# Optimization experiments

Measured on AMD Instinct MI355X. Metric: run time of the kernel, lower is better.

Reference implementation:

```python
import jax, jax.numpy as jnp
import numpy as np


def conv2d_same(x, w, b):
    # x: (B,C,H,W), w: (O,I,3,3) -> 3x3 'same' conv, stride 1
    y = jax.lax.conv_general_dilated(
        x, w, window_strides=(1, 1), padding=((1, 1), (1, 1)),
        dimension_numbers=("NCHW", "OIHW", "NCHW"))
    return y + b[None, :, None, None]


def setup_inputs() -> dict:
    key = jax.random.key(0)
    ks = jax.random.split(key, 7)
    B, F, E, H, W = 16, 64, 16, 64, 64
    fan2d = F * 9
    state = jax.random.normal(ks[0], (B, F, H, W), dtype=jnp.float32)
    pre_w = jax.random.normal(ks[1], (F, F, 3, 3), dtype=jnp.float32) / np.sqrt(fan2d)
    pre_b = jax.random.normal(ks[2], (F,), dtype=jnp.float32) * 0.01
    attn_w = jax.random.normal(ks[3], (E, F, 3, 3), dtype=jnp.float32) / np.sqrt(fan2d)
    attn_b = jax.random.normal(ks[4], (E,), dtype=jnp.float32) * 0.01
    c3_w = jax.random.normal(ks[5], (F, F), dtype=jnp.float32) / np.sqrt(F)
    c3_b = jax.random.normal(ks[6], (F,), dtype=jnp.float32) * 0.01
    return {"state": state, "pre_w": pre_w, "pre_b": pre_b,
            "attn_w": attn_w, "attn_b": attn_b, "c3_w": c3_w, "c3_b": c3_b}


def reference(state, pre_w, pre_b, attn_w, attn_b, c3_w, c3_b):
    # pre_conv + relu
    x = jax.nn.relu(conv2d_same(state, pre_w, pre_b))
    # visattn_conv + sigmoid -> (B,E,H,W)
    attn = jax.nn.sigmoid(conv2d_same(x, attn_w, attn_b))
    # einsum 'bfyx,beyx->bfeyx'
    x5 = state[:, :, None, :, :] * attn[:, None, :, :, :]  # (B,F,E,H,W)
    # Conv3d kernel (1,1,1) with padding (0,1,1): zero-pad H,W by 1,
    # then pointwise linear over F. Output spatial dims become (E, H+2, W+2).
    x5 = jnp.pad(x5, ((0, 0), (0, 0), (0, 0), (1, 1), (1, 1)))
    y = jnp.einsum("of,bfeyx->boeyx", c3_w, x5) + c3_b[None, :, None, None, None]
    y = jax.nn.relu(y)
    # permute (0,2,1,3,4) then mean over last two dims -> (B,E,F)
    out = jnp.mean(y, axis=(-1, -2)).transpose(0, 2, 1)
    return out, attn
```

## Files before the change

kernel.cpp:

```cpp
#include <hip/hip_runtime.h>
#include <math.h>

constexpr int B = 16, F = 64, E = 16, H = 64, W = 64;
constexpr int HW = H * W;
constexpr int XP = 66;
constexpr int CP = 72;
constexpr int YSTRIDE = XP * F;

typedef __bf16 bf16x8 __attribute__((ext_vector_type(8)));
typedef __bf16 bf16x4 __attribute__((ext_vector_type(4)));
typedef float f32x16 __attribute__((ext_vector_type(16)));
typedef float f32x4 __attribute__((ext_vector_type(4)));

__global__ __launch_bounds__(256) void prep_kernel(
    const float* __restrict__ state, const float* __restrict__ pre_w,
    const float* __restrict__ attn_w, const float* __restrict__ c3_w,
    __bf16* __restrict__ xTs, __bf16* __restrict__ wA1,
    __bf16* __restrict__ wA2, __bf16* __restrict__ wT3b,
    float* __restrict__ out0)
{
    __shared__ float s_t[64][68];
    const int blk = blockIdx.x;
    const int tid = threadIdx.x;

    if (blk < 1024) {
        const int b = blk >> 6, y = blk & 63;
        {
            int c = tid >> 2, x0 = (tid & 3) * 16;
            const float* src = state + ((size_t)(b * F + c) * H + y) * W + x0;
            #pragma unroll
            for (int q = 0; q < 4; ++q)
                *(float4*)&s_t[c][x0 + 4 * q] = *(const float4*)(src + 4 * q);
        }
        __syncthreads();
        __bf16* dst = xTs + (size_t)(b * H + y) * YSTRIDE;
        #pragma unroll
        for (int i = 0; i < 2; ++i) {
            int t = tid + i * 256;
            int x = t >> 3, cg = t & 7;
            bf16x8 v;
            #pragma unroll
            for (int j = 0; j < 8; ++j) v[j] = (__bf16)s_t[cg * 8 + j][x];
            *(bf16x8*)(dst + (x + 1) * F + cg * 8) = v;
        }
        if (tid < 16) {
            int bd = tid >> 3, cg = tid & 7;
            bf16x8 z = {};
            *(bf16x8*)(dst + (bd ? 65 : 0) * F + cg * 8) = z;
        }
    } else if (blk < 1168) {
        int idx = (blk - 1024) * 256 + tid;
        if (idx < 64 * 576) {
            int o = idx / 576, rem = idx - o * 576, t = rem >> 6, c = rem & 63;
            wA1[idx] = (__bf16)pre_w[(o * 64 + c) * 9 + t];
        }
        if (idx < 16 * 576) {
            int e = idx / 576, rem = idx - e * 576, t = rem >> 6, c = rem & 63;
            wA2[idx] = (__bf16)attn_w[(e * 64 + c) * 9 + t];
        }
        if (idx < 64 * 64) {
            wT3b[idx] = (__bf16)c3_w[idx];
        }
    } else {
        int idx = (blk - 1168) * 256 + tid;
        float4 z = {0.f, 0.f, 0.f, 0.f};
        *(float4*)(out0 + idx * 4) = z;
    }
}

__global__ __launch_bounds__(256) void conv1_mfma(
    const __bf16* __restrict__ xTs, const __bf16* __restrict__ wA1,
    const float* __restrict__ bias, __bf16* __restrict__ xT1)
{
    __shared__ __bf16 s_x[4 * XP * CP];
    const int b = blockIdx.y, y0 = blockIdx.x * 2;
    const int tid = threadIdx.x;

    for (int t = tid; t < 4 * XP * 8; t += 256) {
        int r = t / (XP * 8);
        int rem = t - r * (XP * 8);
        int x = rem >> 3, cg = rem & 7;
        int yy = y0 - 1 + r;
        bf16x8 v = {};
        if (yy >= 0 && yy < H)
            v = *(const bf16x8*)(xTs + (size_t)(b * H + yy) * YSTRIDE + x * F + cg * 8);
        *(bf16x8*)(s_x + (r * XP + x) * CP + cg * 8) = v;
    }
    __syncthreads();

    const int wave = tid >> 6, lane = tid & 63;
    const int mt = wave & 1;
    const int np = wave >> 1;
    const int n = lane & 31, kh = lane >> 5;
    f32x16 acc0 = {}, acc1 = {};
    const __bf16* aBase = wA1 + (mt * 32 + n) * 576 + kh * 8;

    #pragma unroll
    for (int dy = 0; dy < 3; ++dy) {
        #pragma unroll
        for (int dx = 0; dx < 3; ++dx) {
            const int t9 = dy * 3 + dx;
            const __bf16* bBase = s_x + ((np + dy) * XP + (n + dx)) * CP + kh * 8;
            #pragma unroll
            for (int cq = 0; cq < 4; ++cq) {
                bf16x8 a  = *(const bf16x8*)(aBase + t9 * 64 + cq * 16);
                bf16x8 b0 = *(const bf16x8*)(bBase + cq * 16);
                bf16x8 b1 = *(const bf16x8*)(bBase + 32 * CP + cq * 16);
                acc0 = __builtin_amdgcn_mfma_f32_32x32x16_bf16(a, b0, acc0, 0, 0, 0);
                acc1 = __builtin_amdgcn_mfma_f32_32x32x16_bf16(a, b1, acc1, 0, 0, 0);
            }
        }
    }

    __bf16* obase = xT1 + (size_t)(b * H + y0 + np) * YSTRIDE;
    #pragma unroll
    for (int g = 0; g < 4; ++g) {
        int o0 = mt * 32 + kh * 4 + g * 8;
        f32x4 b4 = *(const f32x4*)(bias + o0);
        bf16x4 v0, v1;
        #pragma unroll
        for (int r = 0; r < 4; ++r) {
            v0[r] = (__bf16)fmaxf(acc0[g * 4 + r] + b4[r], 0.f);
            v1[r] = (__bf16)fmaxf(acc1[g * 4 + r] + b4[r], 0.f);
        }
        *(bf16x4*)(obase + (n + 1) * F + o0) = v0;
        *(bf16x4*)(obase + (n + 33) * F + o0) = v1;
    }
    if (tid < 32) {
        int r2 = tid >> 4, bd = (tid >> 3) & 1, cg = tid & 7;
        bf16x8 z = {};
        *(bf16x8*)(xT1 + (size_t)(b * H + y0 + r2) * YSTRIDE + (bd ? 65 : 0) * F + cg * 8) = z;
    }
}

__global__ __launch_bounds__(256) void conv2_mfma(
    const __bf16* __restrict__ xT1, const __bf16* __restrict__ wA2,
    const float* __restrict__ bias, float* __restrict__ attn)
{
    __shared__ __bf16 s_x[6 * XP * CP];
    const int b = blockIdx.y, y0 = blockIdx.x * 4;
    const int tid = threadIdx.x;

    for (int t = tid; t < 6 * XP * 8; t += 256) {
        int r = t / (XP * 8);
        int rem = t - r * (XP * 8);
        int x = rem >> 3, cg = rem & 7;
        int yy = y0 - 1 + r;
        bf16x8 v = {};
        if (yy >= 0 && yy < H)
            v = *(const bf16x8*)(xT1 + (size_t)(b * H + yy) * YSTRIDE + x * F + cg * 8);
        *(bf16x8*)(s_x + (r * XP + x) * CP + cg * 8) = v;
    }
    __syncthreads();

    const int w = tid >> 6, lane = tid & 63;
    const int n = lane & 15, quad = lane >> 4;
    f32x4 acc[4] = {};
    const __bf16* aBase = wA2 + n * 576 + quad * 8;

    #pragma unroll
    for (int dy = 0; dy < 3; ++dy) {
        #pragma unroll
        for (int dx = 0; dx < 3; ++dx) {
            const int t9 = dy * 3 + dx;
            const __bf16* bBase = s_x + ((w + dy) * XP + (n + dx)) * CP + quad * 8;
            #pragma unroll
            for (int cq = 0; cq < 2; ++cq) {
                bf16x8 a = *(const bf16x8*)(aBase + t9 * 64 + cq * 32);
                #pragma unroll
                for (int i = 0; i < 4; ++i) {
                    bf16x8 bf = *(const bf16x8*)(bBase + (i * 16) * CP + cq * 32);
                    acc[i] = __builtin_amdgcn_mfma_f32_16x16x32_bf16(a, bf, acc[i], 0, 0, 0);
                }
            }
        }
    }

    const int y = y0 + w;
    #pragma unroll
    for (int i = 0; i < 4; ++i) {
        int x = i * 16 + n;
        #pragma unroll
        for (int r = 0; r < 4; ++r) {
            int e = quad * 4 + r;
            float val = acc[i][r] + bias[e];
            attn[((size_t)(b * E + e) * H + y) * W + x] = 1.f / (1.f + __expf(-val));
        }
    }
}

__global__ __launch_bounds__(256) void reduce_fused(
    const __bf16* __restrict__ xTs, const __bf16* __restrict__ wT3b,
    const float* __restrict__ attn, const float* __restrict__ c3_b,
    float* __restrict__ out)
{
    __shared__ __align__(16) float s_attn[64][16];
    __shared__ __align__(16) float s_sp[64][68];
    const int b = blockIdx.y, y = blockIdx.x;
    const int tid = threadIdx.x;

    {
        int e = tid >> 4, pq = (tid & 15) * 4;
        float4 v = *(const float4*)(attn + ((size_t)(b * E + e) * H + y) * W + pq);
        s_attn[pq + 0][e] = v.x; s_attn[pq + 1][e] = v.y;
        s_attn[pq + 2][e] = v.z; s_attn[pq + 3][e] = v.w;
    }

    {
        const int wave = tid >> 6, lane = tid & 63;
        const int mt = wave & 1, nt = wave >> 1;
        const int n = lane & 31, kh = lane >> 5;
        const __bf16* bBase = xTs + (size_t)(b * H + y) * YSTRIDE + (nt * 32 + n + 1) * F + kh * 8;
        const __bf16* aBase = wT3b + (mt * 32 + n) * 64 + kh * 8;
        f32x16 acc = {};
        #pragma unroll
        for (int cq = 0; cq < 4; ++cq) {
            bf16x8 a  = *(const bf16x8*)(aBase + cq * 16);
            bf16x8 bb = *(const bf16x8*)(bBase + cq * 16);
            acc = __builtin_amdgcn_mfma_f32_32x32x16_bf16(a, bb, acc, 0, 0, 0);
        }
        #pragma unroll
        for (int g = 0; g < 4; ++g)
            #pragma unroll
            for (int r = 0; r < 4; ++r)
                s_sp[nt * 32 + n][mt * 32 + kh * 4 + g * 8 + r] = acc[g * 4 + r];
    }
    __syncthreads();

    const int combo = tid & 63;
    const int eg = combo >> 4;
    const int og = combo & 15;
    const int psub = tid >> 6;
    float4 cb4 = ((const float4*)c3_b)[og];
    float cb[4] = {cb4.x, cb4.y, cb4.z, cb4.w};

    float acc[4][4] = {};
    #pragma unroll 2
    for (int pp = 0; pp < 16; ++pp) {
        int p = psub * 16 + pp;
        float4 a4 = *(const float4*)&s_attn[p][eg * 4];
        float4 s4 = *(const float4*)&s_sp[p][og * 4];
        float a[4] = {a4.x, a4.y, a4.z, a4.w};
        float s[4] = {s4.x, s4.y, s4.z, s4.w};
        #pragma unroll
        for (int i = 0; i < 4; ++i)
            #pragma unroll
            for (int j = 0; j < 4; ++j)
                acc[i][j] += fmaxf(fmaf(a[i], s[j], cb[j]), 0.f);
    }

    __syncthreads();
    float* s_part = &s_sp[0][0];
    #pragma unroll
    for (int i = 0; i < 4; ++i)
        #pragma unroll
        for (int j = 0; j < 4; ++j)
            s_part[(psub * 64 + combo) * 16 + i * 4 + j] = acc[i][j];
    __syncthreads();

    {
        int cmb = tid >> 2, i = tid & 3;
        int e = (cmb >> 4) * 4 + i;
        #pragma unroll
        for (int j = 0; j < 4; ++j) {
            int o = (cmb & 15) * 4 + j;
            float v = 0.f;
            #pragma unroll
            for (int ps = 0; ps < 4; ++ps)
                v += s_part[(ps * 64 + cmb) * 16 + i * 4 + j];
            float add = v * (1.f / 4356.f);
            if (y == 0)
                add += 260.f * fmaxf(c3_b[o], 0.f) * (1.f / 4356.f);
            atomicAdd(&out[(b * E + e) * F + o], add);
        }
    }
}

extern "C" void kernel_launch(void* const* d_in, const int* in_sizes, int n_in,
                              void* d_out, int out_size, void* d_ws, size_t ws_size,
                              hipStream_t stream) {
    (void)in_sizes; (void)n_in; (void)out_size; (void)ws_size;
    const float* state  = (const float*)d_in[0];
    const float* pre_w  = (const float*)d_in[1];
    const float* pre_b  = (const float*)d_in[2];
    const float* attn_w = (const float*)d_in[3];
    const float* attn_b = (const float*)d_in[4];
    const float* c3_w   = (const float*)d_in[5];
    const float* c3_b   = (const float*)d_in[6];

    float* out      = (float*)d_out;
    float* attn_out = out + B * E * F;

    char* ws = (char*)d_ws;
    constexpr size_t XT_BYTES = (size_t)B * H * YSTRIDE * 2;
    __bf16* xTs  = (__bf16*)ws;
    __bf16* xT1  = (__bf16*)(ws + XT_BYTES);
    __bf16* wA1  = (__bf16*)(ws + 2 * XT_BYTES);
    __bf16* wA2  = (__bf16*)(ws + 2 * XT_BYTES + 73728);
    __bf16* wT3b = (__bf16*)(ws + 2 * XT_BYTES + 73728 + 18432);

    prep_kernel<<<1184, 256, 0, stream>>>(state, pre_w, attn_w, c3_w,
                                          xTs, wA1, wA2, wT3b, out);
    conv1_mfma<<<dim3(H / 2, B), 256, 0, stream>>>(xTs, wA1, pre_b, xT1);
    conv2_mfma<<<dim3(H / 4, B), 256, 0, stream>>>(xT1, wA2, attn_b, attn_out);
    reduce_fused<<<dim3(H, B), 256, 0, stream>>>(xTs, wT3b, attn_out, c3_b, out);
}
```

Baseline: 126.3 us.

## Fuse all four kernels into one persistent kernel with grid barriers

Replaces the prep, conv1, conv2 and reduce launches with a single 512-block kernel that runs each stage in turn, separated by a software grid barrier built on an atomic counter. Each block owns two rows of one batch, and conv2 keeps its sigmoid attention tile in shared memory for the pointwise-conv reduction instead of reading it back from global memory. This removes three launch gaps and the attention round-trip. In exchange, the kernel relies on all 512 blocks being co-resident (two per CU via launch bounds), and the barrier spins on global atomics.

```diff
diff --git a/kernel.cpp b/kernel.cpp
--- a/kernel.cpp
+++ b/kernel.cpp
@@ -2,7 +2,6 @@
 #include <math.h>
 
 constexpr int B = 16, F = 64, E = 16, H = 64, W = 64;
-constexpr int HW = H * W;
 constexpr int XP = 66;
 constexpr int CP = 72;
 constexpr int YSTRIDE = XP * F;
@@ -12,266 +11,270 @@
 typedef float f32x16 __attribute__((ext_vector_type(16)));
 typedef float f32x4 __attribute__((ext_vector_type(4)));
 
-__global__ __launch_bounds__(256) void prep_kernel(
+__device__ unsigned long long g_bar = 0;
+
+__device__ __forceinline__ void grid_barrier() {
+    __syncthreads();
+    if (threadIdx.x == 0) {
+        __threadfence();
+        unsigned long long ret =
+            __hip_atomic_fetch_add(&g_bar, 1ull, __ATOMIC_ACQ_REL, __HIP_MEMORY_SCOPE_AGENT);
+        unsigned long long target = (ret & ~511ull) + 512ull;
+        while (__hip_atomic_load(&g_bar, __ATOMIC_ACQUIRE, __HIP_MEMORY_SCOPE_AGENT) < target)
+            __builtin_amdgcn_s_sleep(2);
+        __threadfence();
+    }
+    __syncthreads();
+}
+
+__global__ __launch_bounds__(256, 2) void fused_all(
     const float* __restrict__ state, const float* __restrict__ pre_w,
-    const float* __restrict__ attn_w, const float* __restrict__ c3_w,
-    __bf16* __restrict__ xTs, __bf16* __restrict__ wA1,
-    __bf16* __restrict__ wA2, __bf16* __restrict__ wT3b,
-    float* __restrict__ out0)
+    const float* __restrict__ pre_b, const float* __restrict__ attn_w,
+    const float* __restrict__ attn_b, const float* __restrict__ c3_w,
+    const float* __restrict__ c3_b,
+    __bf16* __restrict__ xTs, __bf16* __restrict__ xT1,
+    __bf16* __restrict__ wA1, __bf16* __restrict__ wA2,
+    __bf16* __restrict__ wT3b,
+    float* __restrict__ out, float* __restrict__ attn_out)
 {
-    __shared__ float s_t[64][68];
+    __shared__ __align__(16) char smem[38912];
     const int blk = blockIdx.x;
     const int tid = threadIdx.x;
-
-    if (blk < 1024) {
-        const int b = blk >> 6, y = blk & 63;
+    const int b = blk >> 5, yp = blk & 31;
+    const int wave = tid >> 6, lane = tid & 63;
+
+    {
+        float (*ts)[64][68] = (float(*)[64][68])smem;
         {
             int c = tid >> 2, x0 = (tid & 3) * 16;
-            const float* src = state + ((size_t)(b * F + c) * H + y) * W + x0;
-            #pragma unroll
-            for (int q = 0; q < 4; ++q)
-                *(float4*)&s_t[c][x0 + 4 * q] = *(const float4*)(src + 4 * q);
-        }
-        __syncthreads();
-        __bf16* dst = xTs + (size_t)(b * H + y) * YSTRIDE;
+            #pragma unroll
+            for (int rr = 0; rr < 2; ++rr) {
+                const float* src = state + ((size_t)(b * F + c) * H + (yp * 2 + rr)) * W + x0;
+                #pragma unroll
+                for (int q = 0; q < 4; ++q)
+                    *(float4*)&ts[rr][c][x0 + 4 * q] = *(const float4*)(src + 4 * q);
+            }
+        }
+        __syncthreads();
+        #pragma unroll
+        for (int rr = 0; rr < 2; ++rr) {
+            __bf16* dst = xTs + (size_t)(b * H + yp * 2 + rr) * YSTRIDE;
+            #pragma unroll
+            for (int i = 0; i < 2; ++i) {
+                int t = tid + i * 256;
+                int x = t >> 3, cg = t & 7;
+                bf16x8 v;
+                #pragma unroll
+                for (int j = 0; j < 8; ++j) v[j] = (__bf16)ts[rr][cg * 8 + j][x];
+                *(bf16x8*)(dst + (x + 1) * F + cg * 8) = v;
+            }
+            if (tid < 16) {
+                int bd = tid >> 3, cg = tid & 7;
+                bf16x8 z = {};
+                *(bf16x8*)(dst + (bd ? 65 : 0) * F + cg * 8) = z;
+            }
+        }
+        if (blk < 144) {
+            int idx = blk * 256 + tid;
+            if (idx < 64 * 576) {
+                int o = idx / 576, rem = idx - o * 576, t = rem >> 6, c = rem & 63;
+                wA1[idx] = (__bf16)pre_w[(o * 64 + c) * 9 + t];
+            }
+            if (idx < 16 * 576) {
+                int e = idx / 576, rem = idx - e * 576, t = rem >> 6, c = rem & 63;
+                wA2[idx] = (__bf16)attn_w[(e * 64 + c) * 9 + t];
+            }
+            if (idx < 64 * 64) wT3b[idx] = (__bf16)c3_w[idx];
+        } else if (blk < 160) {
+            int idx = (blk - 144) * 256 + tid;
+            float4 z = {0.f, 0.f, 0.f, 0.f};
+            *(float4*)(out + idx * 4) = z;
+        }
+    }
+    grid_barrier();
+
+    {
+        __bf16* sx = (__bf16*)smem;
+        const int y0 = yp * 2;
+        for (int t = tid; t < 4 * XP * 8; t += 256) {
+            int r = t / (XP * 8), rem = t - r * (XP * 8);
+            int x = rem >> 3, cg = rem & 7;
+            int yy = y0 - 1 + r;
+            bf16x8 v = {};
+            if (yy >= 0 && yy < H)
+                v = *(const bf16x8*)(xTs + (size_t)(b * H + yy) * YSTRIDE + x * F + cg * 8);
+            *(bf16x8*)(sx + (r * XP + x) * CP + cg * 8) = v;
+        }
+        __syncthreads();
+
+        const int mt = wave & 1, np = wave >> 1;
+        const int n = lane & 31, kh = lane >> 5;
+        f32x16 acc0 = {}, acc1 = {};
+        const __bf16* aBase = wA1 + (mt * 32 + n) * 576 + kh * 8;
+        #pragma unroll
+        for (int dy = 0; dy < 3; ++dy)
+            #pragma unroll
+            for (int dx = 0; dx < 3; ++dx) {
+                const int t9 = dy * 3 + dx;
+                const __bf16* bBase = sx + ((np + dy) * XP + (n + dx)) * CP + kh * 8;
+                #pragma unroll
+                for (int cq = 0; cq < 4; ++cq) {
+                    bf16x8 a  = *(const bf16x8*)(aBase + t9 * 64 + cq * 16);
+                    bf16x8 b0 = *(const bf16x8*)(bBase + cq * 16);
+                    bf16x8 b1 = *(const bf16x8*)(bBase + 32 * CP + cq * 16);
+                    acc0 = __builtin_amdgcn_mfma_f32_32x32x16_bf16(a, b0, acc0, 0, 0, 0);
+                    acc1 = __builtin_amdgcn_mfma_f32_32x32x16_bf16(a, b1, acc1, 0, 0, 0);
+                }
+            }
+        __bf16* obase = xT1 + (size_t)(b * H + y0 + np) * YSTRIDE;
+        #pragma unroll
+        for (int g = 0; g < 4; ++g) {
+            int o0 = mt * 32 + kh * 4 + g * 8;
+            f32x4 b4 = *(const f32x4*)(pre_b + o0);
+            bf16x4 v0, v1;
+            #pragma unroll
+            for (int r = 0; r < 4; ++r) {
+                v0[r] = (__bf16)fmaxf(acc0[g * 4 + r] + b4[r], 0.f);
+                v1[r] = (__bf16)fmaxf(acc1[g * 4 + r] + b4[r], 0.f);
+            }
+            *(bf16x4*)(obase + (n + 1) * F + o0) = v0;
+            *(bf16x4*)(obase + (n + 33) * F + o0) = v1;
+        }
+        if (tid < 32) {
+            int r2 = tid >> 4, bd = (tid >> 3) & 1, cg = tid & 7;
+            bf16x8 z = {};
+            *(bf16x8*)(xT1 + (size_t)(b * H + y0 + r2) * YSTRIDE + (bd ? 65 : 0) * F + cg * 8) = z;
+        }
+    }
+    grid_barrier();
+
+    {
+        __bf16* sx = (__bf16*)smem;
+        float (*s_attn)[64][16] = (float(*)[64][16])smem;
+        float (*s_sp)[68] = (float(*)[68])(smem + 8192);
+        const int y0 = yp * 2;
+
+        for (int t = tid; t < 4 * XP * 8; t += 256) {
+            int r = t / (XP * 8), rem = t - r * (XP * 8);
+            int x = rem >> 3, cg = rem & 7;
+            int yy = y0 - 1 + r;
+            bf16x8 v = {};
+            if (yy >= 0 && yy < H)
+                v = *(const bf16x8*)(xT1 + (size_t)(b * H + yy) * YSTRIDE + x * F + cg * 8);
+            *(bf16x8*)(sx + (r * XP + x) * CP + cg * 8) = v;
+        }
+        __syncthreads();
+
+        const int rw = wave >> 1, nt2 = wave & 1;
+        const int n16 = lane & 15, quad = lane >> 4;
+        f32x4 acc2[2] = {};
+        {
+            const __bf16* aB = wA2 + n16 * 576 + quad * 8;
+            #pragma unroll
+            for (int dy = 0; dy < 3; ++dy)
+                #pragma unroll
+                for (int dx = 0; dx < 3; ++dx) {
+                    const int t9 = dy * 3 + dx;
+                    #pragma unroll
+                    for (int cq = 0; cq < 2; ++cq) {
+                        bf16x8 a = *(const bf16x8*)(aB + t9 * 64 + cq * 32);
+                        #pragma unroll
+                        for (int i = 0; i < 2; ++i) {
+                            const __bf16* bp = sx +
+                                ((rw + dy) * XP + (nt2 * 32 + i * 16 + n16 + dx)) * CP
+                                + quad * 8 + cq * 32;
+                            acc2[i] = __builtin_amdgcn_mfma_f32_16x16x32_bf16(
+                                a, *(const bf16x8*)bp, acc2[i], 0, 0, 0);
+                        }
+                    }
+                }
+        }
+        __syncthreads();
+
         #pragma unroll
         for (int i = 0; i < 2; ++i) {
-            int t = tid + i * 256;
-            int x = t >> 3, cg = t & 7;
-            bf16x8 v;
-            #pragma unroll
-            for (int j = 0; j < 8; ++j) v[j] = (__bf16)s_t[cg * 8 + j][x];
-            *(bf16x8*)(dst + (x + 1) * F + cg * 8) = v;
-        }
-        if (tid < 16) {
-            int bd = tid >> 3, cg = tid & 7;
-            bf16x8 z = {};
-            *(bf16x8*)(dst + (bd ? 65 : 0) * F + cg * 8) = z;
-        }
-    } else if (blk < 1168) {
-        int idx = (blk - 1024) * 256 + tid;
-        if (idx < 64 * 576) {
-            int o = idx / 576, rem = idx - o * 576, t = rem >> 6, c = rem & 63;
-            wA1[idx] = (__bf16)pre_w[(o * 64 + c) * 9 + t];
-        }
-        if (idx < 16 * 576) {
-            int e = idx / 576, rem = idx - e * 576, t = rem >> 6, c = rem & 63;
-            wA2[idx] = (__bf16)attn_w[(e * 64 + c) * 9 + t];
-        }
-        if (idx < 64 * 64) {
-            wT3b[idx] = (__bf16)c3_w[idx];
-        }
-    } else {
-        int idx = (blk - 1168) * 256 + tid;
-        float4 z = {0.f, 0.f, 0.f, 0.f};
-        *(float4*)(out0 + idx * 4) = z;
-    }
-}
-
-__global__ __launch_bounds__(256) void conv1_mfma(
-    const __bf16* __restrict__ xTs, const __bf16* __restrict__ wA1,
-    const float* __restrict__ bias, __bf16* __restrict__ xT1)
-{
-    __shared__ __bf16 s_x[4 * XP * CP];
-    const int b = blockIdx.y, y0 = blockIdx.x * 2;
-    const int tid = threadIdx.x;
-
-    for (int t = tid; t < 4 * XP * 8; t += 256) {
-        int r = t / (XP * 8);
-        int rem = t - r * (XP * 8);
-        int x = rem >> 3, cg = rem & 7;
-        int yy = y0 - 1 + r;
-        bf16x8 v = {};
-        if (yy >= 0 && yy < H)
-            v = *(const bf16x8*)(xTs + (size_t)(b * H + yy) * YSTRIDE + x * F + cg * 8);
-        *(bf16x8*)(s_x + (r * XP + x) * CP + cg * 8) = v;
-    }
-    __syncthreads();
-
-    const int wave = tid >> 6, lane = tid & 63;
-    const int mt = wave & 1;
-    const int np = wave >> 1;
-    const int n = lane & 31, kh = lane >> 5;
-    f32x16 acc0 = {}, acc1 = {};
-    const __bf16* aBase = wA1 + (mt * 32 + n) * 576 + kh * 8;
-
-    #pragma unroll
-    for (int dy = 0; dy < 3; ++dy) {
-        #pragma unroll
-        for (int dx = 0; dx < 3; ++dx) {
-            const int t9 = dy * 3 + dx;
-            const __bf16* bBase = s_x + ((np + dy) * XP + (n + dx)) * CP + kh * 8;
-            #pragma unroll
-            for (int cq = 0; cq < 4; ++cq) {
-                bf16x8 a  = *(const bf16x8*)(aBase + t9 * 64 + cq * 16);
-                bf16x8 b0 = *(const bf16x8*)(bBase + cq * 16);
-                bf16x8 b1 = *(const bf16x8*)(bBase + 32 * CP + cq * 16);
-                acc0 = __builtin_amdgcn_mfma_f32_32x32x16_bf16(a, b0, acc0, 0, 0, 0);
-                acc1 = __builtin_amdgcn_mfma_f32_32x32x16_bf16(a, b1, acc1, 0, 0, 0);
-            }
-        }
-    }
-
-    __bf16* obase = xT1 + (size_t)(b * H + y0 + np) * YSTRIDE;
-    #pragma unroll
-    for (int g = 0; g < 4; ++g) {
-        int o0 = mt * 32 + kh * 4 + g * 8;
-        f32x4 b4 = *(const f32x4*)(bias + o0);
-        bf16x4 v0, v1;
-        #pragma unroll
-        for (int r = 0; r < 4; ++r) {
-            v0[r] = (__bf16)fmaxf(acc0[g * 4 + r] + b4[r], 0.f);
-            v1[r] = (__bf16)fmaxf(acc1[g * 4 + r] + b4[r], 0.f);
-        }
-        *(bf16x4*)(obase + (n + 1) * F + o0) = v0;
-        *(bf16x4*)(obase + (n + 33) * F + o0) = v1;
-    }
-    if (tid < 32) {
-        int r2 = tid >> 4, bd = (tid >> 3) & 1, cg = tid & 7;
-        bf16x8 z = {};
-        *(bf16x8*)(xT1 + (size_t)(b * H + y0 + r2) * YSTRIDE + (bd ? 65 : 0) * F + cg * 8) = z;
-    }
-}
-
-__global__ __launch_bounds__(256) void conv2_mfma(
-    const __bf16* __restrict__ xT1, const __bf16* __restrict__ wA2,
-    const float* __restrict__ bias, float* __restrict__ attn)
-{
-    __shared__ __bf16 s_x[6 * XP * CP];
-    const int b = blockIdx.y, y0 = blockIdx.x * 4;
-    const int tid = threadIdx.x;
-
-    for (int t = tid; t < 6 * XP * 8; t += 256) {
-        int r = t / (XP * 8);
-        int rem = t - r * (XP * 8);
-        int x = rem >> 3, cg = rem & 7;
-        int yy = y0 - 1 + r;
-        bf16x8 v = {};
-        if (yy >= 0 && yy < H)
-            v = *(const bf16x8*)(xT1 + (size_t)(b * H + yy) * YSTRIDE + x * F + cg * 8);
-        *(bf16x8*)(s_x + (r * XP + x) * CP + cg * 8) = v;
-    }
-    __syncthreads();
-
-    const int w = tid >> 6, lane = tid & 63;
-    const int n = lane & 15, quad = lane >> 4;
-    f32x4 acc[4] = {};
-    const __bf16* aBase = wA2 + n * 576 + quad * 8;
-
-    #pragma unroll
-    for (int dy = 0; dy < 3; ++dy) {
-        #pragma unroll
-        for (int dx = 0; dx < 3; ++dx) {
-            const int t9 = dy * 3 + dx;
-            const __bf16* bBase = s_x + ((w + dy) * XP + (n + dx)) * CP + quad * 8;
-            #pragma unroll
-            for (int cq = 0; cq < 2; ++cq) {
-                bf16x8 a = *(const bf16x8*)(aBase + t9 * 64 + cq * 32);
-                #pragma unroll
-                for (int i = 0; i < 4; ++i) {
-                    bf16x8 bf = *(const bf16x8*)(bBase + (i * 16) * CP + cq * 32);
-                    acc[i] = __builtin_amdgcn_mfma_f32_16x16x32_bf16(a, bf, acc[i], 0, 0, 0);
+            int x = nt2 * 32 + i * 16 + n16;
+            #pragma unroll
+            for (int r = 0; r < 4; ++r) {
+                int e = quad * 4 + r;
+                float val = acc2[i][r] + attn_b[e];
+                float sg = 1.f / (1.f + __expf(-val));
+                attn_out[((size_t)(b * E + e) * H + (y0 + rw)) * W + x] = sg;
+                s_attn[rw][x][e] = sg;
+            }
+        }
+        __syncthreads();
+
+        const int combo = tid & 63;
+        const int eg = combo >> 4, og = combo & 15, psub = tid >> 6;
+        f32x4 cb4 = ((const f32x4*)c3_b)[og];
+        float vsum[4] = {0.f, 0.f, 0.f, 0.f};
+
+        for (int rr = 0; rr < 2; ++rr) {
+            {
+                const int mt = wave & 1, nt = wave >> 1;
+                const int n = lane & 31, kh = lane >> 5;
+                const __bf16* bBase = xTs + (size_t)(b * H + y0 + rr) * YSTRIDE
+                                      + (nt * 32 + n + 1) * F + kh * 8;
+                const __bf16* aBase = wT3b + (mt * 32 + n) * 64 + kh * 8;
+                f32x16 acc = {};
+                #pragma unroll
+                for (int cq = 0; cq < 4; ++cq) {
+                    bf16x8 a  = *(const bf16x8*)(aBase + cq * 16);
+                    bf16x8 bb = *(const bf16x8*)(bBase + cq * 16);
+                    acc = __builtin_amdgcn_mfma_f32_32x32x16_bf16(a, bb, acc, 0, 0, 0);
                 }
-            }
-        }
-    }
-
-    const int y = y0 + w;
-    #pragma unroll
-    for (int i = 0; i < 4; ++i) {
-        int x = i * 16 + n;
-        #pragma unroll
-        for (int r = 0; r < 4; ++r) {
-            int e = quad * 4 + r;
-            float val = acc[i][r] + bias[e];
-            attn[((size_t)(b * E + e) * H + y) * W + x] = 1.f / (1.f + __expf(-val));
-        }
-    }
-}
-
-__global__ __launch_bounds__(256) void reduce_fused(
-    const __bf16* __restrict__ xTs, const __bf16* __restrict__ wT3b,
-    const float* __restrict__ attn, const float* __restrict__ c3_b,
-    float* __restrict__ out)
-{
-    __shared__ __align__(16) float s_attn[64][16];
-    __shared__ __align__(16) float s_sp[64][68];
-    const int b = blockIdx.y, y = blockIdx.x;
-    const int tid = threadIdx.x;
-
-    {
-        int e = tid >> 4, pq = (tid & 15) * 4;
-        float4 v = *(const float4*)(attn + ((size_t)(b * E + e) * H + y) * W + pq);
-        s_attn[pq + 0][e] = v.x; s_attn[pq + 1][e] = v.y;
-        s_attn[pq + 2][e] = v.z; s_attn[pq + 3][e] = v.w;
-    }
-
-    {
-        const int wave = tid >> 6, lane = tid & 63;
-        const int mt = wave & 1, nt = wave >> 1;
-        const int n = lane & 31, kh = lane >> 5;
-        const __bf16* bBase = xTs + (size_t)(b * H + y) * YSTRIDE + (nt * 32 + n + 1) * F + kh * 8;
-        const __bf16* aBase = wT3b + (mt * 32 + n) * 64 + kh * 8;
-        f32x16 acc = {};
-        #pragma unroll
-        for (int cq = 0; cq < 4; ++cq) {
-            bf16x8 a  = *(const bf16x8*)(aBase + cq * 16);
-            bf16x8 bb = *(const bf16x8*)(bBase + cq * 16);
-            acc = __builtin_amdgcn_mfma_f32_32x32x16_bf16(a, bb, acc, 0, 0, 0);
-        }
-        #pragma unroll
-        for (int g = 0; g < 4; ++g)
-            #pragma unroll
-            for (int r = 0; r < 4; ++r)
-                s_sp[nt * 32 + n][mt * 32 + kh * 4 + g * 8 + r] = acc[g * 4 + r];
-    }
-    __syncthreads();
-
-    const int combo = tid & 63;
-    const int eg = combo >> 4;
-    const int og = combo & 15;
-    const int psub = tid >> 6;
-    float4 cb4 = ((const float4*)c3_b)[og];
-    float cb[4] = {cb4.x, cb4.y, cb4.z, cb4.w};
-
-    float acc[4][4] = {};
-    #pragma unroll 2
-    for (int pp = 0; pp < 16; ++pp) {
-        int p = psub * 16 + pp;
-        float4 a4 = *(const float4*)&s_attn[p][eg * 4];
-        float4 s4 = *(const float4*)&s_sp[p][og * 4];
-        float a[4] = {a4.x, a4.y, a4.z, a4.w};
-        float s[4] = {s4.x, s4.y, s4.z, s4.w};
-        #pragma unroll
-        for (int i = 0; i < 4; ++i)
-            #pragma unroll
-            for (int j = 0; j < 4; ++j)
-                acc[i][j] += fmaxf(fmaf(a[i], s[j], cb[j]), 0.f);
-    }
-
-    __syncthreads();
-    float* s_part = &s_sp[0][0];
-    #pragma unroll
-    for (int i = 0; i < 4; ++i)
-        #pragma unroll
-        for (int j = 0; j < 4; ++j)
-            s_part[(psub * 64 + combo) * 16 + i * 4 + j] = acc[i][j];
-    __syncthreads();
-
-    {
-        int cmb = tid >> 2, i = tid & 3;
-        int e = (cmb >> 4) * 4 + i;
-        #pragma unroll
-        for (int j = 0; j < 4; ++j) {
-            int o = (cmb & 15) * 4 + j;
-            float v = 0.f;
-            #pragma unroll
-            for (int ps = 0; ps < 4; ++ps)
-                v += s_part[(ps * 64 + cmb) * 16 + i * 4 + j];
-            float add = v * (1.f / 4356.f);
-            if (y == 0)
-                add += 260.f * fmaxf(c3_b[o], 0.f) * (1.f / 4356.f);
-            atomicAdd(&out[(b * E + e) * F + o], add);
+                #pragma unroll
+                for (int g = 0; g < 4; ++g)
+                    #pragma unroll
+                    for (int r = 0; r < 4; ++r)
+                        s_sp[nt * 32 + n][mt * 32 + kh * 4 + g * 8 + r] = acc[g * 4 + r];
+            }
+            __syncthreads();
+
+            float accl[4][4] = {};
+            #pragma unroll 2
+            for (int pp = 0; pp < 16; ++pp) {
+                int p = psub * 16 + pp;
+                f32x4 a4 = *(const f32x4*)&s_attn[rr][p][eg * 4];
+                f32x4 s4 = *(const f32x4*)&s_sp[p][og * 4];
+                #pragma unroll
+                for (int i = 0; i < 4; ++i)
+                    #pragma unroll
+                    for (int j = 0; j < 4; ++j)
+                        accl[i][j] += fmaxf(fmaf(a4[i], s4[j], cb4[j]), 0.f);
+            }
+            __syncthreads();
+            float* s_part = &s_sp[0][0];
+            #pragma unroll
+            for (int i = 0; i < 4; ++i)
+                #pragma unroll
+                for (int j = 0; j < 4; ++j)
+                    s_part[(psub * 64 + combo) * 16 + i * 4 + j] = accl[i][j];
+            __syncthreads();
+            {
+                int cmb = tid >> 2, ii = tid & 3;
+                #pragma unroll
+                for (int j = 0; j < 4; ++j) {
+                    float v = 0.f;
+                    #pragma unroll
+                    for (int ps = 0; ps < 4; ++ps)
+                        v += s_part[(ps * 64 + cmb) * 16 + ii * 4 + j];
+                    vsum[j] += v;
+                }
+            }
+            __syncthreads();
+        }
+        {
+            int cmb = tid >> 2, ii = tid & 3;
+            int e = (cmb >> 4) * 4 + ii;
+            #pragma unroll
+            for (int j = 0; j < 4; ++j) {
+                int o = (cmb & 15) * 4 + j;
+                float add = vsum[j] * (1.f / 4356.f);
+                if (yp == 0) add += 260.f * fmaxf(c3_b[o], 0.f) * (1.f / 4356.f);
+                atomicAdd(&out[(b * E + e) * F + o], add);
+            }
         }
     }
 }
@@ -299,9 +302,7 @@
     __bf16* wA2  = (__bf16*)(ws + 2 * XT_BYTES + 73728);
     __bf16* wT3b = (__bf16*)(ws + 2 * XT_BYTES + 73728 + 18432);
 
-    prep_kernel<<<1184, 256, 0, stream>>>(state, pre_w, attn_w, c3_w,
-                                          xTs, wA1, wA2, wT3b, out);
-    conv1_mfma<<<dim3(H / 2, B), 256, 0, stream>>>(xTs, wA1, pre_b, xT1);
-    conv2_mfma<<<dim3(H / 4, B), 256, 0, stream>>>(xT1, wA2, attn_b, attn_out);
-    reduce_fused<<<dim3(H, B), 256, 0, stream>>>(xTs, wT3b, attn_out, c3_b, out);
+    fused_all<<<512, 256, 0, stream>>>(state, pre_w, pre_b, attn_w, attn_b,
+                                       c3_w, c3_b, xTs, xT1, wA1, wA2, wT3b,
+                                       out, attn_out);
 }
```

After: 250.6 us. +98.4%, slower.
